# Kernel optimization log

Measured on AMD Instinct MI355X. Metric: run time of the kernel, lower is better.

## Reference

```python
import math
import jax, jax.numpy as jnp
import numpy as np

D, L, E, O, Q, H, DH, T, B, N, FF = 1024, 8, 768, 1024, 16, 16, 64, 320, 64, 577, 4096
EPS = 1e-5


def layernorm(x, g, b):
    m = jnp.mean(x, axis=-1, keepdims=True)
    v = jnp.var(x, axis=-1, keepdims=True)
    return (x - m) * jax.lax.rsqrt(v + EPS) * g + b


def timestep_sinusoid(t):
    # diffusers Timesteps(320, flip_sin_to_cos=True, freq_shift=0)
    half = T // 2
    freqs = jnp.exp(-math.log(10000.0) * jnp.arange(half, dtype=jnp.float32) / half)
    args = t.astype(jnp.float32)[:, None] * freqs[None, :]
    return jnp.concatenate([jnp.cos(args), jnp.sin(args)], axis=-1)  # flipped order


def setup_inputs() -> dict:
    key = jax.random.key(0)
    ks = iter(jax.random.split(key, 32))
    std = 0.02
    inp = {}
    inp["x"] = jax.random.normal(next(ks), (B, N, E), jnp.float32)
    inp["timestep"] = jax.random.randint(next(ks), (B,), 0, 1000, jnp.int64 if jax.config.jax_enable_x64 else jnp.int32)
    inp["latents"] = jax.random.normal(next(ks), (1, Q, D), jnp.float32) / math.sqrt(D)
    inp["proj_in_w"] = jax.random.normal(next(ks), (D, E), jnp.float32) * std
    inp["proj_in_b"] = jnp.zeros((D,), jnp.float32)
    inp["time_w1"] = jax.random.normal(next(ks), (D, T), jnp.float32) * std
    inp["time_b1"] = jnp.zeros((D,), jnp.float32)
    inp["time_w2"] = jax.random.normal(next(ks), (D, D), jnp.float32) * std
    inp["time_b2"] = jnp.zeros((D,), jnp.float32)
    inp["ln1_g"] = jnp.ones((L, D), jnp.float32)
    inp["ln1_b"] = jnp.zeros((L, D), jnp.float32)
    inp["ln2_g"] = jnp.ones((L, D), jnp.float32)
    inp["ln2_b"] = jnp.zeros((L, D), jnp.float32)
    inp["q_w"] = jax.random.normal(next(ks), (L, D, D), jnp.float32) * std
    inp["kv_w"] = jax.random.normal(next(ks), (L, 2 * D, D), jnp.float32) * std
    inp["out_w"] = jax.random.normal(next(ks), (L, D, D), jnp.float32) * std
    inp["ffln_g"] = jnp.ones((L, D), jnp.float32)
    inp["ffln_b"] = jnp.zeros((L, D), jnp.float32)
    inp["ff_w1"] = jax.random.normal(next(ks), (L, FF, D), jnp.float32) * std
    inp["ff_w2"] = jax.random.normal(next(ks), (L, D, FF), jnp.float32) * std
    inp["ada_w"] = jax.random.normal(next(ks), (L, 4 * D, D), jnp.float32) * std
    inp["ada_b"] = jnp.zeros((L, 4 * D), jnp.float32)
    inp["proj_out_w"] = jax.random.normal(next(ks), (O, D), jnp.float32) * std
    inp["proj_out_b"] = jnp.zeros((O,), jnp.float32)
    inp["nout_g"] = jnp.ones((O,), jnp.float32)
    inp["nout_b"] = jnp.zeros((O,), jnp.float32)
    return inp


def reference(x, timestep, latents, proj_in_w, proj_in_b, time_w1, time_b1, time_w2, time_b2,
              ln1_g, ln1_b, ln2_g, ln2_b, q_w, kv_w, out_w, ffln_g, ffln_b, ff_w1, ff_w2,
              ada_w, ada_b, proj_out_w, proj_out_b, nout_g, nout_b):
    b = x.shape[0]
    # timestep embedding
    t_emb = timestep_sinusoid(timestep).astype(x.dtype)
    temb = jax.nn.silu(t_emb @ time_w1.T + time_b1) @ time_w2.T + time_b2  # [B, D]

    lat = jnp.broadcast_to(latents, (b, Q, D))
    xp = x @ proj_in_w.T + proj_in_b + temb[:, None, :]  # [B, N, D]

    sc = 1.0 / math.sqrt(math.sqrt(DH))
    for i in range(L):
        mod = jax.nn.silu(temb) @ ada_w[i].T + ada_b[i]  # [B, 4D]
        shift_msa, scale_msa, shift_mlp, scale_mlp = jnp.split(mod, 4, axis=-1)

        # PerceiverAttention with AdaLN-modulated latents
        xn = layernorm(xp, ln1_g[i], ln1_b[i])
        lt = layernorm(lat, ln2_g[i], ln2_b[i])
        lt = lt * (1.0 + scale_msa[:, None, :]) + shift_msa[:, None, :]
        q = (lt @ q_w[i].T).reshape(b, Q, H, DH).transpose(0, 2, 1, 3)       # [B,H,Q,DH]
        kv_in = jnp.concatenate([xn, lt], axis=1)                             # [B,N+Q,D]
        kv = kv_in @ kv_w[i].T
        k, v = jnp.split(kv, 2, axis=-1)
        kl = kv_in.shape[1]
        k = k.reshape(b, kl, H, DH).transpose(0, 2, 1, 3)
        v = v.reshape(b, kl, H, DH).transpose(0, 2, 1, 3)
        w = jnp.einsum('bhqd,bhkd->bhqk', q * sc, k * sc)
        w = jax.nn.softmax(w.astype(jnp.float32), axis=-1).astype(q.dtype)
        o = jnp.einsum('bhqk,bhkd->bhqd', w, v).transpose(0, 2, 1, 3).reshape(b, Q, H * DH)
        lat = o @ out_w[i].T + lat

        # FFN with AdaLN modulation after its LayerNorm
        h = layernorm(lat, ffln_g[i], ffln_b[i])
        h = h * (1.0 + scale_mlp[:, None, :]) + shift_mlp[:, None, :]
        h = jax.nn.gelu(h @ ff_w1[i].T, approximate=False)
        lat = h @ ff_w2[i].T + lat

    out = lat @ proj_out_w.T + proj_out_b
    out = layernorm(out, nout_g, nout_b)
    return out
```

## Files before the change

### kernel.cpp

```cpp
#include <hip/hip_runtime.h>
#include <hip/hip_bf16.h>
#include <math.h>

#define B_  64
#define N_  577
#define E_  768
#define D_  1024
#define L_  8
#define Q_  16
#define H_  16
#define DH_ 64
#define T_  320
#define FF_ 4096
#define O_  1024
#define MX_ (B_*N_)
#define KL_ (N_+Q_)
#define BQ_ (B_*Q_)
#define KVOFF ((size_t)B_*H_*KL_*DH_)

typedef unsigned short u16;
typedef __bf16 v8bf __attribute__((ext_vector_type(8)));
typedef float  v4f  __attribute__((ext_vector_type(4)));

__device__ __forceinline__ float bf2f(u16 u){
  union { float f; unsigned int i; } v; v.i = ((unsigned int)u) << 16; return v.f;
}
__device__ __forceinline__ u16 f2bf(float f){
  union { float f; unsigned int i; } v; v.f = f;
  unsigned int x = v.i;
  return (u16)((x + 0x7fffu + ((x >> 16) & 1u)) >> 16);
}

__device__ __forceinline__ void gld16(const u16* g, u16* l){
  __builtin_amdgcn_global_load_lds(
      (const __attribute__((address_space(1))) void*)g,
      (__attribute__((address_space(3))) void*)l, 16, 0, 0);
}

__global__ void k_tsnorm(const int* __restrict__ raw, float* __restrict__ tsf){
  __shared__ int nz;
  int tid = threadIdx.x;
  if (tid == 0) nz = 0;
  __syncthreads();
  if (tid < 32 && raw[2 * tid + 1] != 0) atomicOr(&nz, 1);
  __syncthreads();
  int t = (nz == 0) ? raw[2 * tid] : raw[tid];
  tsf[tid] = (float)t;
}

__global__ void k_f2b(const float* __restrict__ src, u16* __restrict__ dst, long long n4){
  long long i = (long long)blockIdx.x * blockDim.x + threadIdx.x;
  long long stride = (long long)gridDim.x * blockDim.x;
  for (; i < n4; i += stride){
    float4 f = reinterpret_cast<const float4*>(src)[i];
    ushort4 u; u.x = f2bf(f.x); u.y = f2bf(f.y); u.z = f2bf(f.z); u.w = f2bf(f.w);
    reinterpret_cast<ushort4*>(dst)[i] = u;
  }
}

template<int EPI, int BM, int BN>
__global__ __launch_bounds__(256) void k_gemm(
    const u16* __restrict__ X, const u16* __restrict__ Wm,
    const float* __restrict__ bias, const float* __restrict__ aux,
    void* __restrict__ out, void* __restrict__ out2, int M, int N, int K)
{
  constexpr int BK   = 64;
  constexpr int WM   = BM / 2, WN = BN / 2;
  constexpr int MREP = WM / 16, NREP = WN / 16;
  constexpr int NCHA = BM / 8;
  constexpr int NCHB = BN / 8;
  constexpr int NCH  = NCHA + NCHB;
  constexpr int LPW  = NCH / 4;
  constexpr int NBUF = (BM == 128) ? 1 : 2;
  __shared__ u16 As[NBUF * BM * BK];
  __shared__ u16 Bs[NBUF * BN * BK];
  const int tid  = threadIdx.x;
  const int lane = tid & 63;
  const int wid  = tid >> 6;
  const int wr   = wid >> 1, wc = wid & 1;
  const int m0   = blockIdx.y * BM, n0 = blockIdx.x * BN;
  const int fr   = lane & 15;
  const int js   = lane >> 4;
  const int fsw  = (fr >> 1) & 7;

  v4f zero = {0.f, 0.f, 0.f, 0.f};
  v4f acc[MREP][NREP];
  #pragma unroll
  for (int m = 0; m < MREP; ++m)
    #pragma unroll
    for (int n = 0; n < NREP; ++n) acc[m][n] = zero;

  int  aofs[LPW];
  int  loff[LPW];
  bool isAv[LPW];
  #pragma unroll
  for (int p = 0; p < LPW; ++p) {
    const int ch = wid * LPW + p;
    const bool isA = (ch < NCHA);
    const int cb = isA ? ch : ch - NCHA;
    const int fst = (cb * 4 + (lane >> 4)) & 7;
    const int gc  = (((lane & 7) ^ fst) << 3);
    const int grow = cb * 8 + (lane >> 3);
    isAv[p] = isA; loff[p] = cb * 512;
    if (isA) { int ar = m0 + grow; if (ar > M - 1) ar = M - 1; aofs[p] = ar * K + gc; }
    else     { int br = n0 + grow;                              aofs[p] = br * K + gc; }
  }

  auto stage = [&](int buf, int k0){
    const u16* Xk = X + k0;
    const u16* Wk = Wm + k0;
    #pragma unroll
    for (int p = 0; p < LPW; ++p) {
      if (isAv[p]) gld16(Xk + aofs[p], &As[buf * BM * BK + loff[p]]);
      else         gld16(Wk + aofs[p], &Bs[buf * BN * BK + loff[p]]);
    }
  };

  auto compute = [&](const u16* Ab, const u16* Bb){
    if constexpr (BM == 64) __builtin_amdgcn_s_setprio(1);
    #pragma unroll
    for (int kk = 0; kk < 2; ++kk) {
      const int ps = (((kk * 4 + js) ^ fsw) << 3);
      v8bf a[MREP], b[NREP];
      #pragma unroll
      for (int m = 0; m < MREP; ++m)
        a[m] = *reinterpret_cast<const v8bf*>(Ab + (wr * WM + m * 16 + fr) * BK + ps);
      #pragma unroll
      for (int n = 0; n < NREP; ++n)
        b[n] = *reinterpret_cast<const v8bf*>(Bb + (wc * WN + n * 16 + fr) * BK + ps);
      #pragma unroll
      for (int m = 0; m < MREP; ++m)
        #pragma unroll
        for (int n = 0; n < NREP; ++n)
          acc[m][n] = __builtin_amdgcn_mfma_f32_16x16x32_bf16(a[m], b[n], acc[m][n], 0, 0, 0);
    }
    if constexpr (BM == 64) __builtin_amdgcn_s_setprio(0);
  };

  const int nt = K >> 6;
  if constexpr (NBUF == 1) {
    for (int t = 0; t < nt; ++t) {
      stage(0, t << 6);
      __syncthreads();
      compute(&As[0], &Bs[0]);
      __syncthreads();
    }
  } else {
    stage(0, 0);
    for (int t = 0; t < nt; ++t) {
      if (t + 1 < nt) {
        stage((t + 1) & 1, (t + 1) << 6);
        if constexpr (LPW == 4)      asm volatile("s_waitcnt vmcnt(4)" ::: "memory");
        else if constexpr (LPW == 6) asm volatile("s_waitcnt vmcnt(6)" ::: "memory");
        else                         asm volatile("s_waitcnt vmcnt(8)" ::: "memory");
      } else {
        asm volatile("s_waitcnt vmcnt(0)" ::: "memory");
      }
      __builtin_amdgcn_s_barrier();
      compute(&As[(t & 1) * BM * BK], &Bs[(t & 1) * BN * BK]);
      __builtin_amdgcn_s_barrier();
    }
  }

  const int rq = (lane >> 4) << 2;
  #pragma unroll
  for (int m = 0; m < MREP; ++m) {
    #pragma unroll
    for (int r = 0; r < 4; ++r) {
      const int row = m0 + wr * WM + m * 16 + rq + r;
      if (row >= M) continue;
      int bb6 = 0, jj6 = 0;
      if constexpr (EPI == 6) { bb6 = row / N_; jj6 = row - bb6 * N_; }
      #pragma unroll
      for (int n = 0; n < NREP; ++n) {
        const int col = n0 + wc * WN + n * 16 + fr;
        float v = acc[m][n][r];
        if constexpr (EPI == 2 || EPI == 3 || EPI == 6) v += bias[col];
        if constexpr (EPI == 3) v += aux[(size_t)(row / N_) * N + col];
        if constexpr (EPI == 4) v += aux[(size_t)row * N + col];
        if constexpr (EPI == 5) v = 0.5f * v * (1.0f + erff(v * 0.70710678118654752f));
        if constexpr (EPI == 6) {
          int c2 = (col < D_) ? col : col - D_;
          int hh = c2 >> 6, dd = c2 & 63;
          u16* dst = (u16*)out2 + ((col < D_) ? 0 : KVOFF);
          dst[(((size_t)bb6 * H_ + hh) * KL_ + jj6) * DH_ + dd] = f2bf(v);
        } else if constexpr (EPI == 8) {
          if (col < D_) {
            reinterpret_cast<u16*>(out)[(size_t)row * D_ + col] = f2bf(v);
          } else {
            int cc = col - D_;
            int bb = row >> 4, jj = N_ + (row & 15);
            int c2 = (cc < D_) ? cc : cc - D_;
            int hh = c2 >> 6, dd = c2 & 63;
            u16* dst = (u16*)out2 + ((cc < D_) ? 0 : KVOFF);
            dst[(((size_t)bb * H_ + hh) * KL_ + jj) * DH_ + dd] = f2bf(v);
          }
        } else if constexpr (EPI == 2 || EPI == 4) {
          reinterpret_cast<float*>(out)[(size_t)row * N + col] = v;
        } else {
          reinterpret_cast<u16*>(out)[(size_t)row * N + col] = f2bf(v);
        }
      }
    }
  }
}

__global__ __launch_bounds__(256) void k_prep(
    const float* __restrict__ kvw, const float* __restrict__ g, const float* __restrict__ bvec,
    u16* __restrict__ kvf, u16* __restrict__ kvwb, float* __restrict__ kvb,
    const float* __restrict__ qw,  u16* __restrict__ dqw,
    const float* __restrict__ ow,  u16* __restrict__ dow,
    const float* __restrict__ f1w, u16* __restrict__ df1,
    const float* __restrict__ f2w, u16* __restrict__ df2)
{
  __shared__ float sl[4];
  const int bid = blockIdx.x, tid = threadIdx.x;
  if (bid < 2048) {
    int o = bid;
    float4 w = reinterpret_cast<const float4*>(kvw + (size_t)o * D_)[tid];
    float4 gg = reinterpret_cast<const float4*>(g)[tid];
    float4 bv = reinterpret_cast<const float4*>(bvec)[tid];
    ushort4 f;
    f.x = f2bf(w.x * gg.x); f.y = f2bf(w.y * gg.y); f.z = f2bf(w.z * gg.z); f.w = f2bf(w.w * gg.w);
    reinterpret_cast<ushort4*>(kvf + (size_t)o * D_)[tid] = f;
    ushort4 f2;
    f2.x = f2bf(w.x); f2.y = f2bf(w.y); f2.z = f2bf(w.z); f2.w = f2bf(w.w);
    reinterpret_cast<ushort4*>(kvwb + (size_t)o * D_)[tid] = f2;
    float s = w.x * bv.x + w.y * bv.y + w.z * bv.z + w.w * bv.w;
    for (int off = 32; off; off >>= 1) s += __shfl_down(s, off);
    if ((tid & 63) == 0) sl[tid >> 6] = s;
    __syncthreads();
    if (tid == 0) kvb[o] = sl[0] + sl[1] + sl[2] + sl[3];
  } else {
    int id = bid - 2048;
    const float* src; u16* dst; int off;
    if      (id < 1024)  { src = qw;  dst = dqw; off = id; }
    else if (id < 2048)  { src = ow;  dst = dow; off = id - 1024; }
    else if (id < 6144)  { src = f1w; dst = df1; off = id - 2048; }
    else                 { src = f2w; dst = df2; off = id - 6144; }
    size_t base = (size_t)off * 1024 + (size_t)tid * 4;
    float4 v = *reinterpret_cast<const float4*>(src + base);
    ushort4 u; u.x = f2bf(v.x); u.y = f2bf(v.y); u.z = f2bf(v.z); u.w = f2bf(v.w);
    *reinterpret_cast<ushort4*>(dst + base) = u;
  }
}

__global__ void k_temb1(const float* __restrict__ tsf, const float* __restrict__ w1,
                        const float* __restrict__ b1, float* __restrict__ h1tT){
  int o = blockIdx.x, b = threadIdx.x;
  float t = tsf[b];
  float acc = b1[o];
  const float c = -9.210340371976184f / 160.0f;
  for (int j = 0; j < 160; ++j) {
    float arg = t * expf(c * (float)j);
    acc += w1[(size_t)o * T_ + j] * cosf(arg) + w1[(size_t)o * T_ + 160 + j] * sinf(arg);
  }
  float s = acc / (1.0f + expf(-acc));
  h1tT[(size_t)o * B_ + b] = s;
}

__global__ void k_temb2(const float* __restrict__ h1tT, const float* __restrict__ w2,
                        const float* __restrict__ b2, float* __restrict__ temb){
  int o = blockIdx.x, b = threadIdx.x;
  float acc = b2[o];
  for (int d = 0; d < D_; ++d) acc += h1tT[(size_t)d * B_ + b] * w2[(size_t)o * D_ + d];
  temb[(size_t)b * D_ + o] = acc;
}

__global__ void k_silu(const float* __restrict__ in, u16* __restrict__ outb, int n){
  int i = blockIdx.x * blockDim.x + threadIdx.x;
  if (i < n) { float x = in[i]; outb[i] = f2bf(x / (1.0f + expf(-x))); }
}

__global__ void k_init_lat(const float* __restrict__ latents, float* __restrict__ lat){
  int i = blockIdx.x * blockDim.x + threadIdx.x;
  if (i < BQ_ * D_) lat[i] = latents[i & (Q_ * D_ - 1)];
}

__global__ __launch_bounds__(256) void k_rownorm(const u16* __restrict__ xp, u16* __restrict__ outb){
  __shared__ float s1[4], s2[4];
  size_t row = blockIdx.x;
  int tid = threadIdx.x;
  ushort4 u = reinterpret_cast<const ushort4*>(xp + row * D_)[tid];
  float v0 = bf2f(u.x), v1 = bf2f(u.y), v2 = bf2f(u.z), v3 = bf2f(u.w);
  float s = v0 + v1 + v2 + v3;
  float q = v0 * v0 + v1 * v1 + v2 * v2 + v3 * v3;
  for (int off = 32; off; off >>= 1) { s += __shfl_down(s, off); q += __shfl_down(q, off); }
  if ((tid & 63) == 0) { s1[tid >> 6] = s; s2[tid >> 6] = q; }
  __syncthreads();
  float S = s1[0] + s1[1] + s1[2] + s1[3], Qv = s2[0] + s2[1] + s2[2] + s2[3];
  float mean = S * (1.f / D_);
  float rs = rsqrtf(Qv * (1.f / D_) - mean * mean + 1e-5f);
  ushort4 o;
  o.x = f2bf((v0 - mean) * rs); o.y = f2bf((v1 - mean) * rs);
  o.z = f2bf((v2 - mean) * rs); o.w = f2bf((v3 - mean) * rs);
  reinterpret_cast<ushort4*>(outb + row * D_)[tid] = o;
}

__global__ __launch_bounds__(256) void k_lnmod(const float* __restrict__ in, const float* __restrict__ g,
                                               const float* __restrict__ bb, const float* __restrict__ modp,
                                               int mstride, u16* __restrict__ outb){
  __shared__ float s1[4], s2[4];
  int row = blockIdx.x, tid = threadIdx.x;
  int b = row >> 4;
  float4 v = reinterpret_cast<const float4*>(in + (size_t)row * D_)[tid];
  float s = v.x + v.y + v.z + v.w;
  float q = v.x * v.x + v.y * v.y + v.z * v.z + v.w * v.w;
  for (int off = 32; off; off >>= 1) { s += __shfl_down(s, off); q += __shfl_down(q, off); }
  if ((tid & 63) == 0) { s1[tid >> 6] = s; s2[tid >> 6] = q; }
  __syncthreads();
  float S = s1[0] + s1[1] + s1[2] + s1[3], Qv = s2[0] + s2[1] + s2[2] + s2[3];
  float mean = S * (1.f / D_);
  float rs = rsqrtf(Qv * (1.f / D_) - mean * mean + 1e-5f);
  float4 gg = reinterpret_cast<const float4*>(g)[tid];
  float4 bv = reinterpret_cast<const float4*>(bb)[tid];
  const float* mrow = modp + (size_t)b * mstride;
  float4 sh = reinterpret_cast<const float4*>(mrow)[tid];
  float4 scv = reinterpret_cast<const float4*>(mrow + D_)[tid];
  ushort4 o;
  o.x = f2bf(((v.x - mean) * rs * gg.x + bv.x) * (1.f + scv.x) + sh.x);
  o.y = f2bf(((v.y - mean) * rs * gg.y + bv.y) * (1.f + scv.y) + sh.y);
  o.z = f2bf(((v.z - mean) * rs * gg.z + bv.z) * (1.f + scv.z) + sh.z);
  o.w = f2bf(((v.w - mean) * rs * gg.w + bv.w) * (1.f + scv.w) + sh.w);
  reinterpret_cast<ushort4*>(outb + (size_t)row * D_)[tid] = o;
}

__global__ __launch_bounds__(256) void k_lnfinal(const float* __restrict__ in, const float* __restrict__ g,
                                                 const float* __restrict__ bb, float* __restrict__ outf){
  __shared__ float s1[4], s2[4];
  int row = blockIdx.x, tid = threadIdx.x;
  float4 v = reinterpret_cast<const float4*>(in + (size_t)row * O_)[tid];
  float s = v.x + v.y + v.z + v.w;
  float q = v.x * v.x + v.y * v.y + v.z * v.z + v.w * v.w;
  for (int off = 32; off; off >>= 1) { s += __shfl_down(s, off); q += __shfl_down(q, off); }
  if ((tid & 63) == 0) { s1[tid >> 6] = s; s2[tid >> 6] = q; }
  __syncthreads();
  float S = s1[0] + s1[1] + s1[2] + s1[3], Qv = s2[0] + s2[1] + s2[2] + s2[3];
  float mean = S * (1.f / O_);
  float rs = rsqrtf(Qv * (1.f / O_) - mean * mean + 1e-5f);
  float4 gg = reinterpret_cast<const float4*>(g)[tid];
  float4 bv = reinterpret_cast<const float4*>(bb)[tid];
  float4 o;
  o.x = (v.x - mean) * rs * gg.x + bv.x;
  o.y = (v.y - mean) * rs * gg.y + bv.y;
  o.z = (v.z - mean) * rs * gg.z + bv.z;
  o.w = (v.w - mean) * rs * gg.w + bv.w;
  reinterpret_cast<float4*>(outf + (size_t)row * O_)[tid] = o;
}

__global__ __launch_bounds__(256) void k_attn2(const u16* __restrict__ qb,
                                               const u16* __restrict__ kb,
                                               const u16* __restrict__ vb,
                                               u16* __restrict__ ob){
  __shared__ float qs[Q_][DH_ + 4];
  __shared__ u16   ks[128][DH_ + 4];
  __shared__ float sc[Q_][600];
  __shared__ float rsum[Q_];
  const int bh  = blockIdx.x;
  const int b   = bh >> 4, h = bh & 15;
  const int tid = threadIdx.x;
  {
    int qi = tid >> 4, d4 = (tid & 15) << 2;
    ushort4 u = *reinterpret_cast<const ushort4*>(qb + (size_t)(b * Q_ + qi) * D_ + h * DH_ + d4);
    qs[qi][d4 + 0] = 0.125f * bf2f(u.x);
    qs[qi][d4 + 1] = 0.125f * bf2f(u.y);
    qs[qi][d4 + 2] = 0.125f * bf2f(u.z);
    qs[qi][d4 + 3] = 0.125f * bf2f(u.w);
  }
  const u16* kbh = kb + (size_t)bh * KL_ * DH_;
  const u16* vbh = vb + (size_t)bh * KL_ * DH_;
  for (int j0 = 0; j0 < KL_; j0 += 128) {
    int rows = KL_ - j0; if (rows > 128) rows = 128;
    __syncthreads();
    for (int idx = tid; idx < rows * 16; idx += 256) {
      int r = idx >> 4, c4 = (idx & 15) << 2;
      *reinterpret_cast<ushort4*>(&ks[r][c4]) =
          *reinterpret_cast<const ushort4*>(kbh + (size_t)(j0 + r) * DH_ + c4);
    }
    __syncthreads();
    for (int e = tid; e < Q_ * 128; e += 256) {
      int jj = e & 127, qi = e >> 7;
      if (jj < rows) {
        float s = 0.f;
        #pragma unroll
        for (int d = 0; d < DH_; d += 4) {
          ushort4 u = *reinterpret_cast<const ushort4*>(&ks[jj][d]);
          s += qs[qi][d] * bf2f(u.x) + qs[qi][d + 1] * bf2f(u.y)
             + qs[qi][d + 2] * bf2f(u.z) + qs[qi][d + 3] * bf2f(u.w);
        }
        sc[qi][j0 + jj] = s;
      }
    }
  }
  __syncthreads();
  {
    int g = tid >> 4, l = tid & 15;
    float mx = -1e30f;
    for (int j = l; j < KL_; j += 16) mx = fmaxf(mx, sc[g][j]);
    for (int m = 1; m < 16; m <<= 1) mx = fmaxf(mx, __shfl_xor(mx, m));
    float sum = 0.f;
    for (int j = l; j < KL_; j += 16) { float e = expf(sc[g][j] - mx); sc[g][j] = e; sum += e; }
    for (int m = 1; m < 16; m <<= 1) sum += __shfl_xor(sum, m);
    if (l == 0) rsum[g] = sum;
  }
  {
    int d = tid & 63, q0 = tid >> 6;
    float acc[4] = {0.f, 0.f, 0.f, 0.f};
    for (int j0 = 0; j0 < KL_; j0 += 128) {
      int rows = KL_ - j0; if (rows > 128) rows = 128;
      __syncthreads();
      for (int idx = tid; idx < rows * 16; idx += 256) {
        int r = idx >> 4, c4 = (idx & 15) << 2;
        *reinterpret_cast<ushort4*>(&ks[r][c4]) =
            *reinterpret_cast<const ushort4*>(vbh + (size_t)(j0 + r) * DH_ + c4);
      }
      __syncthreads();
      for (int jj = 0; jj < rows; ++jj) {
        float vj = bf2f(ks[jj][d]);
        #pragma unroll
        for (int t = 0; t < 4; ++t) acc[t] += sc[q0 + t * 4][j0 + jj] * vj;
      }
    }
    #pragma unroll
    for (int t = 0; t < 4; ++t) {
      int qi = q0 + t * 4;
      ob[(size_t)(b * Q_ + qi) * D_ + h * DH_ + d] = f2bf(acc[t] / rsum[qi]);
    }
  }
}

static void conv_launch(const float* src, u16* dst, size_t n, hipStream_t s){
  long long n4 = (long long)(n >> 2);
  int blocks = (int)((n4 + 255) / 256);
  if (blocks > 4096) blocks = 4096;
  k_f2b<<<blocks, 256, 0, s>>>(src, dst, n4);
}

template<int EPI, int BM, int BN>
static void gemm(const u16* X, const u16* W, const float* bias, const float* aux,
                 void* out, void* out2, int M, int N, int K, hipStream_t s){
  dim3 g(N / BN, (M + BM - 1) / BM);
  k_gemm<EPI, BM, BN><<<g, 256, 0, s>>>(X, W, bias, aux, out, out2, M, N, K);
}

extern "C" void kernel_launch(void* const* d_in, const int* in_sizes, int n_in,
                              void* d_out, int out_size, void* d_ws, size_t ws_size,
                              hipStream_t stream)
{
  const float* x         = (const float*)d_in[0];
  const int*   tsp       = (const int*)  d_in[1];
  const float* latents   = (const float*)d_in[2];
  const float* proj_in_w = (const float*)d_in[3];
  const float* proj_in_b = (const float*)d_in[4];
  const float* time_w1   = (const float*)d_in[5];
  const float* time_b1   = (const float*)d_in[6];
  const float* time_w2   = (const float*)d_in[7];
  const float* time_b2   = (const float*)d_in[8];
  const float* ln1_g     = (const float*)d_in[9];
  const float* ln1_b     = (const float*)d_in[10];
  const float* ln2_g     = (const float*)d_in[11];
  const float* ln2_b     = (const float*)d_in[12];
  const float* q_w       = (const float*)d_in[13];
  const float* kv_w      = (const float*)d_in[14];
  const float* out_w     = (const float*)d_in[15];
  const float* ffln_g    = (const float*)d_in[16];
  const float* ffln_b    = (const float*)d_in[17];
  const float* ff_w1     = (const float*)d_in[18];
  const float* ff_w2     = (const float*)d_in[19];
  const float* ada_w     = (const float*)d_in[20];
  const float* ada_b     = (const float*)d_in[21];
  const float* proj_out_w= (const float*)d_in[22];
  const float* proj_out_b= (const float*)d_in[23];
  const float* nout_g    = (const float*)d_in[24];
  const float* nout_b    = (const float*)d_in[25];

  char* Wp = (char*)d_ws;
  size_t off = 0;
  auto alloc = [&](size_t bytes) -> void* {
    void* p = Wp + off;
    off = (off + bytes + 255) & ~(size_t)255;
    return p;
  };

  float* tsf   = (float*)alloc((size_t)B_ * 4);
  float* temb  = (float*)alloc((size_t)B_ * D_ * 4);
  float* h1tT  = (float*)alloc((size_t)D_ * B_ * 4);
  u16*   stemb = (u16*)  alloc((size_t)B_ * D_ * 2);
  float* modb8 = (float*)alloc((size_t)B_ * L_ * 4 * D_ * 4);
  float* kvb   = (float*)alloc((size_t)2 * D_ * 4);
  float* lat   = (float*)alloc((size_t)BQ_ * D_ * 4);
  u16*   lt    = (u16*)  alloc((size_t)BQ_ * D_ * 2);
  u16*   qb    = (u16*)  alloc((size_t)BQ_ * D_ * 2);
  u16*   ob    = (u16*)  alloc((size_t)BQ_ * D_ * 2);
  u16*   hb    = (u16*)  alloc((size_t)BQ_ * D_ * 2);
  u16*   h1b   = (u16*)  alloc((size_t)BQ_ * FF_ * 2);
  u16*   latb  = (u16*)  alloc((size_t)BQ_ * D_ * 2);
  float* tmpf  = (float*)alloc((size_t)BQ_ * D_ * 4);
  u16*   wpin  = (u16*)  alloc((size_t)D_ * E_ * 2);
  u16*   wada8 = (u16*)  alloc((size_t)L_ * 4 * D_ * D_ * 2);
  u16*   wpout = (u16*)  alloc((size_t)O_ * D_ * 2);
  u16*   kvf   = (u16*)  alloc((size_t)2 * D_ * D_ * 2);
  u16*   wqkv  = (u16*)  alloc((size_t)3 * D_ * D_ * 2);
  u16*   wouti = (u16*)  alloc((size_t)D_ * D_ * 2);
  u16*   wff1i = (u16*)  alloc((size_t)FF_ * D_ * 2);
  u16*   wff2i = (u16*)  alloc((size_t)D_ * FF_ * 2);
  u16*   nxp   = (u16*)  alloc((size_t)MX_ * D_ * 2);
  u16*   kvwb  = wqkv + (size_t)D_ * D_;
  size_t xb_sz  = (size_t)B_ * N_ * E_ * 2;
  size_t xpb_sz = (size_t)MX_ * D_ * 2;
  size_t kv_sz  = (size_t)B_ * H_ * KL_ * DH_ * 2;
  size_t big_sz = (xb_sz + xpb_sz > 2 * kv_sz) ? (xb_sz + xpb_sz) : 2 * kv_sz;
  char* big = (char*)alloc(big_sz);
  u16* xb   = (u16*)big;
  u16* xpb  = (u16*)(big + xb_sz);
  u16* kbuf = (u16*)big;
  u16* vbuf = (u16*)(big + kv_sz);

  conv_launch(x,          xb,    (size_t)B_ * N_ * E_, stream);
  conv_launch(proj_in_w,  wpin,  (size_t)D_ * E_,      stream);
  conv_launch(proj_out_w, wpout, (size_t)O_ * D_,      stream);
  conv_launch(ada_w,      wada8, (size_t)L_ * 4 * D_ * D_, stream);

  k_tsnorm<<<1, B_, 0, stream>>>(tsp, tsf);
  k_temb1<<<D_, B_, 0, stream>>>(tsf, time_w1, time_b1, h1tT);
  k_temb2<<<D_, B_, 0, stream>>>(h1tT, time_w2, time_b2, temb);
  k_silu<<<(B_ * D_ + 255) / 256, 256, 0, stream>>>(temb, stemb, B_ * D_);

  gemm<2, 64, 64>(stemb, wada8, ada_b, nullptr, modb8, nullptr, B_, L_ * 4 * D_, D_, stream);

  gemm<3, 128, 128>(xb, wpin, proj_in_b, temb, xpb, nullptr, MX_, D_, E_, stream);
  k_rownorm<<<MX_, 256, 0, stream>>>(xpb, nxp);
  k_init_lat<<<(BQ_ * D_) / 256, 256, 0, stream>>>(latents, lat);

  const int MSTR = L_ * 4 * D_;
  for (int i = 0; i < L_; ++i) {
    k_prep<<<12288, 256, 0, stream>>>(
        kv_w + (size_t)i * 2 * D_ * D_, ln1_g + i * D_, ln1_b + i * D_,
        kvf, kvwb, kvb,
        q_w   + (size_t)i * D_ * D_,  wqkv,
        out_w + (size_t)i * D_ * D_,  wouti,
        ff_w1 + (size_t)i * FF_ * D_, wff1i,
        ff_w2 + (size_t)i * D_ * FF_, wff2i);

    gemm<6, 128, 128>(nxp, kvf, kvb, nullptr, nullptr, kbuf, MX_, 2 * D_, D_, stream);
    k_lnmod<<<BQ_, 256, 0, stream>>>(lat, ln2_g + i * D_, ln2_b + i * D_,
                                     modb8 + (size_t)i * 4 * D_, MSTR, lt);
    gemm<8, 64, 64>(lt, wqkv, nullptr, nullptr, qb, kbuf, BQ_, 3 * D_, D_, stream);
    k_attn2<<<B_ * H_, 256, 0, stream>>>(qb, kbuf, vbuf, ob);
    gemm<4, 64, 64>(ob, wouti, nullptr, lat, lat, nullptr, BQ_, D_, D_, stream);
    k_lnmod<<<BQ_, 256, 0, stream>>>(lat, ffln_g + i * D_, ffln_b + i * D_,
                                     modb8 + (size_t)i * 4 * D_ + 2 * D_, MSTR, hb);
    gemm<5, 64, 64>(hb,  wff1i, nullptr, nullptr, h1b, nullptr, BQ_, FF_, D_,  stream);
    gemm<4, 64, 64>(h1b, wff2i, nullptr, lat,     lat, nullptr, BQ_, D_,  FF_, stream);
  }

  conv_launch(lat, latb, (size_t)BQ_ * D_, stream);
  gemm<2, 64, 64>(latb, wpout, proj_out_b, nullptr, tmpf, nullptr, BQ_, O_, D_, stream);
  k_lnfinal<<<BQ_, 256, 0, stream>>>(tmpf, nout_g, nout_b, (float*)d_out);
}
```

Baseline: 3.808 ms.

## Triple-buffer the 128x128 GEMM with BK=32 and two-stage prefetch

The 128x128 GEMM tile used a single LDS buffer with BK=64, so each k-step loaded and then computed with no overlap. It now uses BK=32 with three LDS buffers and keeps two stages of async global-to-LDS loads in flight while computing. The swizzle and load-address mapping are adapted to 32-wide rows. This is meant to hide global memory latency on the large projection and KV GEMMs. The cost is more LDS per block, which may lower occupancy, and twice as many barriers per unit of K.

New measurement: 3.724 ms. -2.2%, faster.

```diff
diff --git a/kernel.cpp b/kernel.cpp
--- a/kernel.cpp
+++ b/kernel.cpp
@@ -64,14 +64,15 @@
     const float* __restrict__ bias, const float* __restrict__ aux,
     void* __restrict__ out, void* __restrict__ out2, int M, int N, int K)
 {
-  constexpr int BK   = 64;
+  constexpr int BK   = (BM == 128) ? 32 : 64;
   constexpr int WM   = BM / 2, WN = BN / 2;
   constexpr int MREP = WM / 16, NREP = WN / 16;
-  constexpr int NCHA = BM / 8;
-  constexpr int NCHB = BN / 8;
+  constexpr int RPC  = 512 / BK;
+  constexpr int NCHA = BM / RPC;
+  constexpr int NCHB = BN / RPC;
   constexpr int NCH  = NCHA + NCHB;
   constexpr int LPW  = NCH / 4;
-  constexpr int NBUF = (BM == 128) ? 1 : 2;
+  constexpr int NBUF = (BM == 128) ? 3 : 2;
   __shared__ u16 As[NBUF * BM * BK];
   __shared__ u16 Bs[NBUF * BN * BK];
   const int tid  = threadIdx.x;
@@ -81,7 +82,7 @@
   const int m0   = blockIdx.y * BM, n0 = blockIdx.x * BN;
   const int fr   = lane & 15;
   const int js   = lane >> 4;
-  const int fsw  = (fr >> 1) & 7;
+  const int fsw  = (fr >> 1) & ((BK == 32) ? 3 : 7);
 
   v4f zero = {0.f, 0.f, 0.f, 0.f};
   v4f acc[MREP][NREP];
@@ -98,9 +99,16 @@
     const int ch = wid * LPW + p;
     const bool isA = (ch < NCHA);
     const int cb = isA ? ch : ch - NCHA;
-    const int fst = (cb * 4 + (lane >> 4)) & 7;
-    const int gc  = (((lane & 7) ^ fst) << 3);
-    const int grow = cb * 8 + (lane >> 3);
+    int grow, gc;
+    if constexpr (BK == 32) {
+      grow = cb * 16 + (lane >> 2);
+      const int fst = (lane >> 3) & 3;
+      gc = (((lane & 3) ^ fst) << 3);
+    } else {
+      grow = cb * 8 + (lane >> 3);
+      const int fst = (cb * 4 + (lane >> 4)) & 7;
+      gc = (((lane & 7) ^ fst) << 3);
+    }
     isAv[p] = isA; loff[p] = cb * 512;
     if (isA) { int ar = m0 + grow; if (ar > M - 1) ar = M - 1; aofs[p] = ar * K + gc; }
     else     { int br = n0 + grow;                              aofs[p] = br * K + gc; }
@@ -119,7 +127,7 @@
   auto compute = [&](const u16* Ab, const u16* Bb){
     if constexpr (BM == 64) __builtin_amdgcn_s_setprio(1);
     #pragma unroll
-    for (int kk = 0; kk < 2; ++kk) {
+    for (int kk = 0; kk < BK / 32; ++kk) {
       const int ps = (((kk * 4 + js) ^ fsw) << 3);
       v8bf a[MREP], b[NREP];
       #pragma unroll
@@ -137,22 +145,32 @@
     if constexpr (BM == 64) __builtin_amdgcn_s_setprio(0);
   };
 
-  const int nt = K >> 6;
-  if constexpr (NBUF == 1) {
+  const int nt = K / BK;
+  if constexpr (NBUF == 3) {
+    stage(0, 0);
+    stage(1, BK);
+    int bi = 0;
     for (int t = 0; t < nt; ++t) {
-      stage(0, t << 6);
-      __syncthreads();
-      compute(&As[0], &Bs[0]);
-      __syncthreads();
+      if (t + 2 < nt) {
+        int sb = bi + 2; if (sb >= 3) sb -= 3;
+        stage(sb, (t + 2) * BK);
+        asm volatile("s_waitcnt vmcnt(8)" ::: "memory");
+      } else if (t + 1 < nt) {
+        asm volatile("s_waitcnt vmcnt(4)" ::: "memory");
+      } else {
+        asm volatile("s_waitcnt vmcnt(0)" ::: "memory");
+      }
+      __builtin_amdgcn_s_barrier();
+      compute(&As[bi * BM * BK], &Bs[bi * BN * BK]);
+      __builtin_amdgcn_s_barrier();
+      ++bi; if (bi == 3) bi = 0;
     }
   } else {
     stage(0, 0);
     for (int t = 0; t < nt; ++t) {
       if (t + 1 < nt) {
-        stage((t + 1) & 1, (t + 1) << 6);
-        if constexpr (LPW == 4)      asm volatile("s_waitcnt vmcnt(4)" ::: "memory");
-        else if constexpr (LPW == 6) asm volatile("s_waitcnt vmcnt(6)" ::: "memory");
-        else                         asm volatile("s_waitcnt vmcnt(8)" ::: "memory");
+        stage((t + 1) & 1, (t + 1) * BK);
+        asm volatile("s_waitcnt vmcnt(4)" ::: "memory");
       } else {
         asm volatile("s_waitcnt vmcnt(0)" ::: "memory");
       }
@@ -546,7 +564,7 @@
     k_lnmod<<<BQ_, 256, 0, stream>>>(lat, ln2_g + i * D_, ln2_b + i * D_,
                                      modb8 + (size_t)i * 4 * D_, MSTR, lt);
     gemm<8, 64, 64>(lt, wqkv, nullptr, nullptr, qb, kbuf, BQ_, 3 * D_, D_, stream);
-    k_attn2<<<B_ * H_, 256, 0, stream>>>(qb, kbuf, vbuf, ob);
+    k_attn2<<<B_ * H_, 0 + 256, 0, stream>>>(qb, kbuf, vbuf, ob);
     gemm<4, 64, 64>(ob, wouti, nullptr, lat, lat, nullptr, BQ_, D_, D_, stream);
     k_lnmod<<<BQ_, 256, 0, stream>>>(lat, ffln_g + i * D_, ffln_b + i * D_,
                                      modb8 + (size_t)i * 4 * D_ + 2 * D_, MSTR, hb);
```
